# Kernel optimization log

Hardware: AMD Instinct MI355X
Metric: run time of the kernel (lower is better)

## Reference

```python
import jax, jax.numpy as jnp
import numpy as np

DILATIONS = (1, 2, 4, 8)
K = 3  # kernel_size
B, H, W, C = 16, 128, 128, 64
HID = 256
OUT = 64  # == C, so residual path is taken


def _depthwise(x, w, dilation):
    # x: [B,H,W,C], w: [K,K,1,C] (HWIO depthwise kernel)
    pad = dilation * (K // 2)
    return jax.lax.conv_general_dilated(
        x, w,
        window_strides=(1, 1),
        padding=[(pad, pad), (pad, pad)],
        rhs_dilation=(dilation, dilation),
        dimension_numbers=('NHWC', 'HWIO', 'NHWC'),
        feature_group_count=C,
    )


def setup_inputs() -> dict:
    key = jax.random.key(0)
    k_x, k_cw, k_w1, k_b1, k_w2, k_b2 = jax.random.split(key, 6)
    in_feat = C * (1 + len(DILATIONS))  # 320
    x = jax.random.normal(k_x, (B, H, W, C), jnp.float32)
    # depthwise kernels, one [K,K,1,C] per dilation, stacked
    conv_w = jax.random.normal(k_cw, (len(DILATIONS), K, K, 1, C), jnp.float32) * (1.0 / np.sqrt(K * K).astype(np.float32))
    W1 = jax.random.normal(k_w1, (in_feat, HID), jnp.float32) * np.float32(1.0 / np.sqrt(in_feat))
    b1 = jax.random.normal(k_b1, (HID,), jnp.float32) * 0.01
    W2 = jax.random.normal(k_w2, (HID, OUT), jnp.float32) * np.float32(1.0 / np.sqrt(HID))
    b2 = jax.random.normal(k_b2, (OUT,), jnp.float32) * 0.01
    return {"x": x, "conv_w": conv_w, "W1": W1, "b1": b1, "W2": W2, "b2": b2}


def reference(x, conv_w, W1, b1, W2, b2):
    # 1) Perception: multiscale depthwise dilated convs (same-padding per dilation)
    perceptions = [_depthwise(x, conv_w[i], d) for i, d in enumerate(DILATIONS)]
    upd_in = jnp.concatenate([x] + perceptions, axis=-1)  # [B,H,W,5C]
    # 2) Update MLP: Linear -> Dropout(eval: identity) -> GELU(exact erf) -> Linear
    h = jax.nn.gelu(upd_in @ W1 + b1, approximate=False)  # [B,H,W,HID]
    delta = h @ W2 + b2  # [B,H,W,OUT]
    # 3) out_channels == channels and (eval mode or fire_rate==1.0): plain residual
    return x + delta
```

## Files before the change

### kernel.cpp

```cpp
#include <hip/hip_runtime.h>
#include <cstdint>

#define B_   16
#define H_   128
#define W_   128
#define C_   64
#define HID_ 256
#define XELEMS (B_ * H_ * W_ * C_)

typedef _Float16 __attribute__((ext_vector_type(2))) half2v;
typedef _Float16 __attribute__((ext_vector_type(8))) half8v;
typedef __attribute__((ext_vector_type(4))) float f32x4;
typedef unsigned short ushort_t;

#define W1S_OFF 0
#define W2S_OFF 81920
#define CWH_OFF 98304
#define XH_OFF  100608
#define FEAT_OFF (XH_OFF + XELEMS)
#define FEAT_HALVES (4096ull * 16384ull)
#define WS_NEED_FULL (2ull * (FEAT_OFF + FEAT_HALVES))

__device__ __forceinline__ int hs(int row, int col) {
  return row * 256 + (((col >> 3) ^ (row & 7)) << 3) + (col & 7);
}

__device__ __forceinline__ float fast_gelu(float h) {
  float u = h * fmaf(h * h, 0.10293921f, 2.30211813f);
  float e = exp2f(-u);
  return h * __builtin_amdgcn_rcpf(1.0f + e);
}

__global__ void prep_kernel(const float* __restrict__ x,
                            const float* __restrict__ W1,
                            const float* __restrict__ W2,
                            const float* __restrict__ cw,
                            _Float16* __restrict__ wsb) {
  if (blockIdx.x < 393) {
    int t = blockIdx.x * 256 + threadIdx.x;
    if (t < 81920) {
      int j = t & 7, lane = (t >> 3) & 63, n16 = (t >> 9) & 15, ks = t >> 13;
      int k = ks * 32 + (lane >> 4) * 8 + j;
      int n = n16 * 16 + (lane & 15);
      wsb[W1S_OFF + t] = (_Float16)W1[k * 256 + n];
    } else if (t < 98304) {
      int t2 = t - 81920;
      int j = t2 & 7, lane = (t2 >> 3) & 63, n16 = (t2 >> 9) & 3, ks = t2 >> 11;
      int k = ks * 32 + (lane >> 4) * 8 + j;
      int n = n16 * 16 + (lane & 15);
      wsb[W2S_OFF + t2] = (_Float16)W2[k * 64 + n];
    } else if (t < 98304 + 2304) {
      int t3 = t - 98304;
      wsb[CWH_OFF + t3] = (_Float16)cw[t3];
    }
  } else {
    int i = ((blockIdx.x - 393) * 256 + threadIdx.x) * 8;
    const float4 a = *(const float4*)&x[i];
    const float4 b = *(const float4*)&x[i + 4];
    half8v o = {(_Float16)a.x, (_Float16)a.y, (_Float16)a.z, (_Float16)a.w,
                (_Float16)b.x, (_Float16)b.y, (_Float16)b.z, (_Float16)b.w};
    *(half8v*)&wsb[XH_OFF + i] = o;
  }
}

__global__ void conv_feat_kernel(const _Float16* __restrict__ xh,
                                 const _Float16* __restrict__ cwh,
                                 _Float16* __restrict__ feat) {
  const int tid   = threadIdx.x;
  const int tileX = blockIdx.x * 8;
  const int tileY = blockIdx.y * 8;
  const int batch = blockIdx.z >> 2;
  const int dd    = blockIdx.z & 3;
  const int dil   = 1 << dd;

  const _Float16* xhb = xh + (size_t)batch * (H_ * W_ * C_);
  _Float16* ft =
      feat + ((size_t)((batch * 16 + blockIdx.y) * 16 + blockIdx.x)) * 16384;

  const int quad = tid & 15;
  const int p0   = tid >> 4;
  const int ksq  = quad >> 3;
  const int c32  = (quad & 7) * 4;

  half2v w01[9], w23[9];
#pragma unroll
  for (int t = 0; t < 9; ++t) {
    uint2 wr = *(const uint2*)&cwh[(dd * 9 + t) * C_ + quad * 4];
    w01[t] = __builtin_bit_cast(half2v, wr.x);
    w23[t] = __builtin_bit_cast(half2v, wr.y);
  }

  uint2 v[4][9];
  const bool interior = (tileX >= 8) && (tileX <= W_ - 16) &&
                        (tileY >= 8) && (tileY <= H_ - 16);
  if (interior) {
#pragma unroll
    for (int i = 0; i < 4; ++i) {
      const int p  = i * 16 + p0;
      const int y0 = tileY + (p >> 3), x0 = tileX + (p & 7);
#pragma unroll
      for (int ky = 0; ky < 3; ++ky)
#pragma unroll
        for (int kx = 0; kx < 3; ++kx)
          v[i][ky * 3 + kx] = *(const uint2*)
              &xhb[((y0 + (ky - 1) * dil) * W_ + x0 + (kx - 1) * dil) * C_ +
                   quad * 4];
    }
  } else {
#pragma unroll
    for (int i = 0; i < 4; ++i) {
      const int p  = i * 16 + p0;
      const int y0 = tileY + (p >> 3), x0 = tileX + (p & 7);
#pragma unroll
      for (int ky = 0; ky < 3; ++ky)
#pragma unroll
        for (int kx = 0; kx < 3; ++kx) {
          const int yy = y0 + (ky - 1) * dil;
          const int xx = x0 + (kx - 1) * dil;
          uint2 vv = {0u, 0u};
          if ((unsigned)yy < (unsigned)H_ && (unsigned)xx < (unsigned)W_)
            vv = *(const uint2*)&xhb[(yy * W_ + xx) * C_ + quad * 4];
          v[i][ky * 3 + kx] = vv;
        }
    }
  }

#pragma unroll
  for (int i = 0; i < 4; ++i) {
    const int p = i * 16 + p0;
    half2v a01 = {0, 0}, a23 = {0, 0};
#pragma unroll
    for (int t = 0; t < 9; ++t) {
      a01 += __builtin_bit_cast(half2v, v[i][t].x) * w01[t];
      a23 += __builtin_bit_cast(half2v, v[i][t].y) * w23[t];
    }
    uint2 pk;
    pk.x = __builtin_bit_cast(uint32_t, a01);
    pk.y = __builtin_bit_cast(uint32_t, a23);
    *(uint2*)&ft[(dd * 2 + ksq) * 2048 + p * 32 + c32] = pk;
  }
}

__global__ __launch_bounds__(256, 2)
void mlp_kernel(const _Float16* __restrict__ xh,
                const _Float16* __restrict__ feat,
                const float* __restrict__ b1,
                const float* __restrict__ b2,
                const _Float16* __restrict__ w1s,
                const _Float16* __restrict__ w2s,
                float* __restrict__ out) {
  __shared__ __align__(16) ushort_t smem[64 * 256];

  const int tid   = threadIdx.x;
  const int tileX = blockIdx.x * 8;
  const int tileY = blockIdx.y * 8;
  const int batch = blockIdx.z;
  const _Float16* xhb = xh + (size_t)batch * (H_ * W_ * C_);
  const _Float16* ftb =
      feat + ((size_t)((batch * 16 + blockIdx.y) * 16 + blockIdx.x)) * 16384;

  const int lane = tid & 63;
  const int wv   = tid >> 6;
  const int lr   = lane & 15;
  const int lg   = lane >> 4;
  const int n0   = wv * 64;

  const half8v* w1v = (const half8v*)w1s;

  half8v xf[4][2];
#pragma unroll
  for (int pi = 0; pi < 4; ++pi) {
    const int p  = pi * 16 + lr;
    const int gp = (tileY + (p >> 3)) * W_ + tileX + (p & 7);
#pragma unroll
    for (int ks = 0; ks < 2; ++ks)
      xf[pi][ks] = *(const half8v*)&xhb[gp * C_ + ks * 32 + lg * 8];
  }

#define LOAD_STEP(FB, WB, S)                                                   \
  do {                                                                         \
    _Pragma("unroll") for (int pi = 0; pi < 4; ++pi)                           \
        FB[pi] = *(const half8v*)&ftb[(S)*2048 + (pi * 16 + lr) * 32 + lg * 8];\
    _Pragma("unroll") for (int hi = 0; hi < 4; ++hi)                           \
        WB[hi] = w1v[(((S) + 2) * 16 + wv * 4 + hi) * 64 + lane];              \
  } while (0)

#define MFMA_STEP(FB, WB)                                                      \
  do {                                                                         \
    _Pragma("unroll") for (int hi = 0; hi < 4; ++hi)                           \
        _Pragma("unroll") for (int pi = 0; pi < 4; ++pi)                       \
        acc[hi][pi] = __builtin_amdgcn_mfma_f32_16x16x32_f16(                  \
            WB[hi], FB[pi], acc[hi][pi], 0, 0, 0);                             \
  } while (0)

  f32x4 acc[4][4];
#pragma unroll
  for (int hi = 0; hi < 4; ++hi)
#pragma unroll
    for (int pi = 0; pi < 4; ++pi) acc[hi][pi] = 0;

  half8v fA[4], wA[4], fB[4], wB[4];
  LOAD_STEP(fA, wA, 0);
  LOAD_STEP(fB, wB, 1);

#pragma unroll
  for (int ks = 0; ks < 2; ++ks) {
    half8v wf[4];
#pragma unroll
    for (int hi = 0; hi < 4; ++hi)
      wf[hi] = w1v[(ks * 16 + wv * 4 + hi) * 64 + lane];
#pragma unroll
    for (int hi = 0; hi < 4; ++hi)
#pragma unroll
      for (int pi = 0; pi < 4; ++pi)
        acc[hi][pi] = __builtin_amdgcn_mfma_f32_16x16x32_f16(
            wf[hi], xf[pi][ks], acc[hi][pi], 0, 0, 0);
  }

  MFMA_STEP(fA, wA); LOAD_STEP(fA, wA, 2);
  MFMA_STEP(fB, wB); LOAD_STEP(fB, wB, 3);
  MFMA_STEP(fA, wA); LOAD_STEP(fA, wA, 4);
  MFMA_STEP(fB, wB); LOAD_STEP(fB, wB, 5);
  MFMA_STEP(fA, wA); LOAD_STEP(fA, wA, 6);
  MFMA_STEP(fB, wB); LOAD_STEP(fB, wB, 7);
  MFMA_STEP(fA, wA);
  MFMA_STEP(fB, wB);

  float4 bias1[4];
#pragma unroll
  for (int hi = 0; hi < 4; ++hi)
    bias1[hi] = *(const float4*)&b1[n0 + hi * 16 + lg * 4];

#pragma unroll
  for (int hi = 0; hi < 4; ++hi) {
#pragma unroll
    for (int pi = 0; pi < 4; ++pi) {
      _Float16 g[4];
#pragma unroll
      for (int q = 0; q < 4; ++q)
        g[q] = (_Float16)fast_gelu(acc[hi][pi][q] + bias1[hi][q]);
      half2v g01 = {g[0], g[1]}, g23 = {g[2], g[3]};
      uint2 pk;
      pk.x = __builtin_bit_cast(uint32_t, g01);
      pk.y = __builtin_bit_cast(uint32_t, g23);
      *(uint2*)&smem[hs(pi * 16 + lr, n0 + hi * 16 + lg * 4)] = pk;
    }
  }
  __syncthreads();

  const int m0 = wv * 16;
  f32x4 acc2[4];
#pragma unroll
  for (int ni = 0; ni < 4; ++ni) acc2[ni] = 0;

  const half8v* w2v = (const half8v*)w2s;
#pragma unroll 2
  for (int ks = 0; ks < 8; ++ks) {
    half8v a2 = *(const half8v*)&smem[hs(m0 + lr, ks * 32 + lg * 8)];
#pragma unroll
    for (int ni = 0; ni < 4; ++ni) {
      half8v bfr = w2v[(ks * 4 + ni) * 64 + lane];
      acc2[ni] = __builtin_amdgcn_mfma_f32_16x16x32_f16(a2, bfr, acc2[ni],
                                                        0, 0, 0);
    }
  }

#pragma unroll
  for (int ni = 0; ni < 4; ++ni) {
    const int col  = ni * 16 + lr;
    const float bias = b2[col];
#pragma unroll
    for (int q = 0; q < 4; ++q) {
      const int row = m0 + lg * 4 + q;
      const int py = row >> 3, px = row & 7;
      const size_t idx =
          ((size_t)(batch * H_ + tileY + py) * W_ + (tileX + px)) * C_ + col;
      out[idx] = (float)xh[idx] + acc2[ni][q] + bias;
    }
  }
}

template <bool BOUND>
__device__ __forceinline__ void conv_phase_f32(const float* __restrict__ xb,
                                               const _Float16* __restrict__ cwh,
                                               ushort_t* __restrict__ feat,
                                               int tid, int tileX, int tileY) {
  const int quad = tid & 15;
  const int p0   = tid >> 4;
#pragma unroll
  for (int dd = 0; dd < 4; ++dd) {
    const int dil = 1 << dd;
    half2v w01[9], w23[9];
#pragma unroll
    for (int t = 0; t < 9; ++t) {
      uint2 wr = *(const uint2*)&cwh[(dd * 9 + t) * C_ + quad * 4];
      w01[t] = __builtin_bit_cast(half2v, wr.x);
      w23[t] = __builtin_bit_cast(half2v, wr.y);
    }
#pragma unroll
    for (int i = 0; i < 4; ++i) {
      const int p  = i * 16 + p0;
      const int y0 = tileY + (p >> 3), x0 = tileX + (p & 7);
      half2v a01 = {0, 0}, a23 = {0, 0};
#pragma unroll
      for (int ky = 0; ky < 3; ++ky) {
        const int yy = y0 + (ky - 1) * dil;
        if (BOUND && (unsigned)yy >= (unsigned)H_) continue;
#pragma unroll
        for (int kx = 0; kx < 3; ++kx) {
          const int xx = x0 + (kx - 1) * dil;
          if (BOUND && (unsigned)xx >= (unsigned)W_) continue;
          const int t = ky * 3 + kx;
          const float4 xv = *(const float4*)&xb[(yy * W_ + xx) * C_ + quad * 4];
          half2v xl = {(_Float16)xv.x, (_Float16)xv.y};
          half2v xh2 = {(_Float16)xv.z, (_Float16)xv.w};
          a01 += xl * w01[t];
          a23 += xh2 * w23[t];
        }
      }
      uint2 pk;
      pk.x = __builtin_bit_cast(uint32_t, a01);
      pk.y = __builtin_bit_cast(uint32_t, a23);
      *(uint2*)&feat[hs(p, dd * 64 + quad * 4)] = pk;
    }
  }
}

__global__ __launch_bounds__(256, 4)
void nca_fused_fp32(const float* __restrict__ x,
                    const _Float16* __restrict__ cwh,
                    const float* __restrict__ b1,
                    const float* __restrict__ b2,
                    const _Float16* __restrict__ w1s,
                    const _Float16* __restrict__ w2s,
                    float* __restrict__ out) {
  __shared__ __align__(16) ushort_t smem[64 * 256];

  const int tid   = threadIdx.x;
  const int tileX = blockIdx.x * 8;
  const int tileY = blockIdx.y * 8;
  const int batch = blockIdx.z;
  const float* xb = x + (size_t)batch * (H_ * W_ * C_);

  const int lane = tid & 63;
  const int wv   = tid >> 6;
  const int lr   = lane & 15;
  const int lg   = lane >> 4;
  const int n0   = wv * 64;

  half8v xf[4][2];
#pragma unroll
  for (int pi = 0; pi < 4; ++pi) {
    const int p  = pi * 16 + lr;
    const int gp = (tileY + (p >> 3)) * W_ + tileX + (p & 7);
#pragma unroll
    for (int ks = 0; ks < 2; ++ks) {
      const float* bp = &xb[gp * C_ + ks * 32 + lg * 8];
      float4 u = *(const float4*)bp, v = *(const float4*)(bp + 4);
      half8v s = {(_Float16)u.x, (_Float16)u.y, (_Float16)u.z, (_Float16)u.w,
                  (_Float16)v.x, (_Float16)v.y, (_Float16)v.z, (_Float16)v.w};
      xf[pi][ks] = s;
    }
  }

  const bool interior = (tileX >= 8) && (tileX <= W_ - 16) &&
                        (tileY >= 8) && (tileY <= H_ - 16);
  if (interior)
    conv_phase_f32<false>(xb, cwh, smem, tid, tileX, tileY);
  else
    conv_phase_f32<true>(xb, cwh, smem, tid, tileX, tileY);
  __syncthreads();

  f32x4 acc[4][4];
#pragma unroll
  for (int hi = 0; hi < 4; ++hi)
#pragma unroll
    for (int pi = 0; pi < 4; ++pi) acc[hi][pi] = 0;

  const half8v* w1v = (const half8v*)w1s;
#pragma unroll
  for (int ks = 0; ks < 2; ++ks) {
    half8v wf[4];
#pragma unroll
    for (int hi = 0; hi < 4; ++hi)
      wf[hi] = w1v[(ks * 16 + wv * 4 + hi) * 64 + lane];
#pragma unroll
    for (int hi = 0; hi < 4; ++hi)
#pragma unroll
      for (int pi = 0; pi < 4; ++pi)
        acc[hi][pi] = __builtin_amdgcn_mfma_f32_16x16x32_f16(
            wf[hi], xf[pi][ks], acc[hi][pi], 0, 0, 0);
  }
  for (int ks = 2; ks < 10; ++ks) {
    half8v ff[4], wf[4];
#pragma unroll
    for (int pi = 0; pi < 4; ++pi)
      ff[pi] = *(const half8v*)&smem[hs(pi * 16 + lr, (ks - 2) * 32 + lg * 8)];
#pragma unroll
    for (int hi = 0; hi < 4; ++hi)
      wf[hi] = w1v[(ks * 16 + wv * 4 + hi) * 64 + lane];
#pragma unroll
    for (int hi = 0; hi < 4; ++hi)
#pragma unroll
      for (int pi = 0; pi < 4; ++pi)
        acc[hi][pi] = __builtin_amdgcn_mfma_f32_16x16x32_f16(
            wf[hi], ff[pi], acc[hi][pi], 0, 0, 0);
  }

  float4 bias1[4];
#pragma unroll
  for (int hi = 0; hi < 4; ++hi)
    bias1[hi] = *(const float4*)&b1[n0 + hi * 16 + lg * 4];

  __syncthreads();

#pragma unroll
  for (int hi = 0; hi < 4; ++hi) {
#pragma unroll
    for (int pi = 0; pi < 4; ++pi) {
      _Float16 g[4];
#pragma unroll
      for (int q = 0; q < 4; ++q)
        g[q] = (_Float16)fast_gelu(acc[hi][pi][q] + bias1[hi][q]);
      half2v g01 = {g[0], g[1]}, g23 = {g[2], g[3]};
      uint2 pk;
      pk.x = __builtin_bit_cast(uint32_t, g01);
      pk.y = __builtin_bit_cast(uint32_t, g23);
      *(uint2*)&smem[hs(pi * 16 + lr, n0 + hi * 16 + lg * 4)] = pk;
    }
  }
  __syncthreads();

  const int m0 = wv * 16;
  f32x4 acc2[4];
#pragma unroll
  for (int ni = 0; ni < 4; ++ni) acc2[ni] = 0;

  const half8v* w2v = (const half8v*)w2s;
  for (int ks = 0; ks < 8; ++ks) {
    half8v a2 = *(const half8v*)&smem[hs(m0 + lr, ks * 32 + lg * 8)];
#pragma unroll
    for (int ni = 0; ni < 4; ++ni) {
      half8v bfr = w2v[(ks * 4 + ni) * 64 + lane];
      acc2[ni] = __builtin_amdgcn_mfma_f32_16x16x32_f16(a2, bfr, acc2[ni],
                                                        0, 0, 0);
    }
  }

#pragma unroll
  for (int ni = 0; ni < 4; ++ni) {
    const int col  = ni * 16 + lr;
    const float bias = b2[col];
#pragma unroll
    for (int q = 0; q < 4; ++q) {
      const int row = m0 + lg * 4 + q;
      const int py = row >> 3, px = row & 7;
      const size_t idx =
          ((size_t)(batch * H_ + tileY + py) * W_ + (tileX + px)) * C_ + col;
      out[idx] = x[idx] + acc2[ni][q] + bias;
    }
  }
}

extern "C" void kernel_launch(void* const* d_in, const int* in_sizes, int n_in,
                              void* d_out, int out_size, void* d_ws,
                              size_t ws_size, hipStream_t stream) {
  const float* x  = (const float*)d_in[0];
  const float* cw = (const float*)d_in[1];
  const float* W1 = (const float*)d_in[2];
  const float* b1 = (const float*)d_in[3];
  const float* W2 = (const float*)d_in[4];
  const float* b2 = (const float*)d_in[5];
  float* out = (float*)d_out;

  _Float16* wsb  = (_Float16*)d_ws;
  _Float16* w1s  = wsb + W1S_OFF;
  _Float16* w2s  = wsb + W2S_OFF;
  _Float16* cwh  = wsb + CWH_OFF;
  _Float16* xh   = wsb + XH_OFF;
  _Float16* feat = wsb + FEAT_OFF;

  dim3 grid(W_ / 8, H_ / 8, B_);

  if (ws_size >= (size_t)WS_NEED_FULL) {
    prep_kernel<<<393 + XELEMS / 8 / 256, 256, 0, stream>>>(x, W1, W2, cw, wsb);
    dim3 cgrid(W_ / 8, H_ / 8, B_ * 4);
    conv_feat_kernel<<<cgrid, 256, 0, stream>>>(xh, cwh, feat);
    mlp_kernel<<<grid, 256, 0, stream>>>(xh, feat, b1, b2, w1s, w2s, out);
  } else {
    prep_kernel<<<393, 256, 0, stream>>>(x, W1, W2, cw, wsb);
    nca_fused_fp32<<<grid, 256, 0, stream>>>(x, cwh, b1, b2, w1s, w2s, out);
  }
}
```

Measured before the change: 208.9 us.

## Stage perception features into LDS via direct global-to-LDS loads in MLP kernel

New measurement: 194.4 us. 6.9% less time.

```diff
diff --git a/kernel.cpp b/kernel.cpp
--- a/kernel.cpp
+++ b/kernel.cpp
@@ -29,6 +29,12 @@
   float u = h * fmaf(h * h, 0.10293921f, 2.30211813f);
   float e = exp2f(-u);
   return h * __builtin_amdgcn_rcpf(1.0f + e);
+}
+
+__device__ __forceinline__ void stage16(const _Float16* g, ushort_t* l) {
+  __builtin_amdgcn_global_load_lds(
+      (const __attribute__((address_space(1))) void*)g,
+      (__attribute__((address_space(3))) void*)l, 16, 0, 0);
 }
 
 __global__ void prep_kernel(const float* __restrict__ x,
@@ -141,7 +147,7 @@
   }
 }
 
-__global__ __launch_bounds__(256, 2)
+__global__ __launch_bounds__(256, 4)
 void mlp_kernel(const _Float16* __restrict__ xh,
                 const _Float16* __restrict__ feat,
                 const float* __restrict__ b1,
@@ -177,31 +183,18 @@
       xf[pi][ks] = *(const half8v*)&xhb[gp * C_ + ks * 32 + lg * 8];
   }
 
-#define LOAD_STEP(FB, WB, S)                                                   \
-  do {                                                                         \
-    _Pragma("unroll") for (int pi = 0; pi < 4; ++pi)                           \
-        FB[pi] = *(const half8v*)&ftb[(S)*2048 + (pi * 16 + lr) * 32 + lg * 8];\
-    _Pragma("unroll") for (int hi = 0; hi < 4; ++hi)                           \
-        WB[hi] = w1v[(((S) + 2) * 16 + wv * 4 + hi) * 64 + lane];              \
-  } while (0)
-
-#define MFMA_STEP(FB, WB)                                                      \
-  do {                                                                         \
-    _Pragma("unroll") for (int hi = 0; hi < 4; ++hi)                           \
-        _Pragma("unroll") for (int pi = 0; pi < 4; ++pi)                       \
-        acc[hi][pi] = __builtin_amdgcn_mfma_f32_16x16x32_f16(                  \
-            WB[hi], FB[pi], acc[hi][pi], 0, 0, 0);                             \
-  } while (0)
+  {
+    const _Float16* src0 = &ftb[(wv * 16 + (lane & 15)) * 32 + (lane >> 4) * 8];
+#pragma unroll
+    for (int s = 0; s < 8; ++s)
+      stage16(src0 + s * 2048, &smem[(s * 4 + wv) * 512]);
+  }
 
   f32x4 acc[4][4];
 #pragma unroll
   for (int hi = 0; hi < 4; ++hi)
 #pragma unroll
     for (int pi = 0; pi < 4; ++pi) acc[hi][pi] = 0;
-
-  half8v fA[4], wA[4], fB[4], wB[4];
-  LOAD_STEP(fA, wA, 0);
-  LOAD_STEP(fB, wB, 1);
 
 #pragma unroll
   for (int ks = 0; ks < 2; ++ks) {
@@ -217,19 +210,39 @@
             wf[hi], xf[pi][ks], acc[hi][pi], 0, 0, 0);
   }
 
-  MFMA_STEP(fA, wA); LOAD_STEP(fA, wA, 2);
-  MFMA_STEP(fB, wB); LOAD_STEP(fB, wB, 3);
-  MFMA_STEP(fA, wA); LOAD_STEP(fA, wA, 4);
-  MFMA_STEP(fB, wB); LOAD_STEP(fB, wB, 5);
-  MFMA_STEP(fA, wA); LOAD_STEP(fA, wA, 6);
-  MFMA_STEP(fB, wB); LOAD_STEP(fB, wB, 7);
-  MFMA_STEP(fA, wA);
-  MFMA_STEP(fB, wB);
+  __syncthreads();
+
+#define LOAD_W(WB, S)                                                         \
+  _Pragma("unroll") for (int hi = 0; hi < 4; ++hi)                            \
+      WB[hi] = w1v[((S) * 16 + wv * 4 + hi) * 64 + lane];
+#define LOAD_F(FB, S)                                                         \
+  _Pragma("unroll") for (int pi = 0; pi < 4; ++pi)                            \
+      FB[pi] = *(const half8v*)&smem[(((S) - 2) * 4 + pi) * 512 + lane * 8];
+#define MFMA16(WB, FB)                                                        \
+  _Pragma("unroll") for (int hi = 0; hi < 4; ++hi)                            \
+      _Pragma("unroll") for (int pi = 0; pi < 4; ++pi)                        \
+      acc[hi][pi] = __builtin_amdgcn_mfma_f32_16x16x32_f16(                   \
+          WB[hi], FB[pi], acc[hi][pi], 0, 0, 0);
+
+  {
+    half8v wfA[4], wfB[4], fA[4];
+    LOAD_W(wfA, 2);
+    LOAD_F(fA, 2); LOAD_W(wfB, 3); MFMA16(wfA, fA);
+    LOAD_F(fA, 3); LOAD_W(wfA, 4); MFMA16(wfB, fA);
+    LOAD_F(fA, 4); LOAD_W(wfB, 5); MFMA16(wfA, fA);
+    LOAD_F(fA, 5); LOAD_W(wfA, 6); MFMA16(wfB, fA);
+    LOAD_F(fA, 6); LOAD_W(wfB, 7); MFMA16(wfA, fA);
+    LOAD_F(fA, 7); LOAD_W(wfA, 8); MFMA16(wfB, fA);
+    LOAD_F(fA, 8); LOAD_W(wfB, 9); MFMA16(wfA, fA);
+    LOAD_F(fA, 9);                 MFMA16(wfB, fA);
+  }
 
   float4 bias1[4];
 #pragma unroll
   for (int hi = 0; hi < 4; ++hi)
     bias1[hi] = *(const float4*)&b1[n0 + hi * 16 + lg * 4];
+
+  __syncthreads();
 
 #pragma unroll
   for (int hi = 0; hi < 4; ++hi) {
@@ -278,6 +291,9 @@
       out[idx] = (float)xh[idx] + acc2[ni][q] + bias;
     }
   }
+#undef LOAD_W
+#undef LOAD_F
+#undef MFMA16
 }
 
 template <bool BOUND>
```
